# Optimization experiments

Hardware: AMD Instinct MI355X
Metric: run time of the kernel (lower is better)

## Reference

```python
import jax, jax.numpy as jnp
import numpy as np

N, NFEAT, NHID, NCLASS, NHEADS = 3072, 128, 64, 64, 8
ALPHA = 0.2  # LeakyReLU negative slope
NEG = -9e15  # masking value from pyGAT


def gat_layer(h, mask, W, a):
    # h: [N, Fin]; mask: [N, N] bool; W: [H, Fin, Fout]; a: [H, 2*Fout]
    fout = W.shape[-1]
    Wh = jnp.einsum('ni,hio->hno', h, W)            # [H, N, Fout]
    e_src = jnp.einsum('hno,ho->hn', Wh, a[:, :fout])
    e_dst = jnp.einsum('hno,ho->hn', Wh, a[:, fout:])
    e = jax.nn.leaky_relu(e_src[:, :, None] + e_dst[:, None, :], ALPHA)  # [H,N,N]
    e = jnp.where(mask[None], e, NEG)
    att = jax.nn.softmax(e, axis=-1)                 # dropout is identity in eval
    out = jnp.einsum('hnm,hmo->hno', att, Wh)        # [H, N, Fout]
    out = jax.nn.elu(out)                            # concat=True -> elu
    # concat heads along feature dim: [N, H*Fout]
    return out.transpose(1, 0, 2).reshape(h.shape[0], -1)


def setup_inputs() -> dict:
    key = jax.random.key(0)
    ks = jax.random.split(key, 10)
    x = jax.random.normal(ks[0], (N, NFEAT), dtype=jnp.float32)
    adj = (jax.random.uniform(ks[1], (N, N)) < 0.01).astype(jnp.float32)
    adj = jnp.maximum(adj, jnp.eye(N, dtype=jnp.float32))
    hid = NHID * NHEADS
    dims = [(NFEAT, NHID), (hid, NHID), (hid, NHID), (hid, NCLASS)]
    params = {}
    for i, (fin, fout) in enumerate(dims):
        kw, ka = jax.random.split(ks[2 + i])
        params[f'W{i+1}'] = jax.random.normal(kw, (NHEADS, fin, fout), dtype=jnp.float32) * (1.0 / np.sqrt(fin))
        params[f'a{i+1}'] = jax.random.normal(ka, (NHEADS, 2 * fout), dtype=jnp.float32) * 0.1
    return {'x': x, 'adj': adj, **params}


def reference(x, adj, W1, a1, W2, a2, W3, a3, W4, a4):
    mask = adj > 0
    h = gat_layer(x, mask, W1, a1)
    h = gat_layer(h, mask, W2, a2)
    h = gat_layer(h, mask, W3, a3)
    h = gat_layer(h, mask, W4, a4)
    return h  # [N, NHEADS*NCLASS]
```

## Files before the change

kernel.cpp:

```cpp
#include <hip/hip_runtime.h>
#include <math.h>

#define NN 3072
#define NH 8
#define FO 64
#define FCAT 512
#define MAXDEG 128
#define ALPHA 0.2f

typedef __attribute__((ext_vector_type(8))) short bf16x8;
typedef __attribute__((ext_vector_type(4))) float f32x4;

static __device__ __forceinline__ unsigned short f2bf(float v) {
    union { float f; unsigned u; } x; x.f = v;
    unsigned r = x.u + 0x7fffu + ((x.u >> 16) & 1u);
    return (unsigned short)(r >> 16);
}
static __device__ __forceinline__ float bf2f(unsigned short b) {
    union { unsigned u; float f; } x; x.u = ((unsigned)b) << 16;
    return x.f;
}

__global__ __launch_bounds__(64) void build_csr_k(const float* __restrict__ adj,
                                                  int* __restrict__ deg,
                                                  int* __restrict__ nbr) {
    int row = blockIdx.x;
    int lane = threadIdx.x;
    const float* arow = adj + (size_t)row * NN;
    int count = 0;
    for (int base = 0; base < NN; base += 64) {
        float v = arow[base + lane];
        unsigned long long m = __ballot(v > 0.0f);
        if (v > 0.0f) {
            int pos = count + __popcll(m & ((1ull << lane) - 1ull));
            if (pos < MAXDEG) nbr[(size_t)row * MAXDEG + pos] = base + lane;
        }
        count += __popcll(m);
    }
    if (lane == 0) deg[row] = count < MAXDEG ? count : MAXDEG;
}

__global__ __launch_bounds__(256) void conv_x_k(const float* __restrict__ x,
                                                unsigned short* __restrict__ xh,
                                                unsigned short* __restrict__ xl, int n) {
    int i = blockIdx.x * 256 + threadIdx.x;
    if (i < n) {
        float v = x[i];
        unsigned short hb = f2bf(v);
        xh[i] = hb;
        xl[i] = f2bf(v - bf2f(hb));
    }
}

__global__ __launch_bounds__(256) void conv_wt_k(const float* __restrict__ W1,
                                                 const float* __restrict__ W2,
                                                 const float* __restrict__ W3,
                                                 const float* __restrict__ W4,
                                                 unsigned short* __restrict__ Wth,
                                                 unsigned short* __restrict__ Wtl) {
    __shared__ float t[64][65];
    int b = blockIdx.x;
    const float* W; int K; int local; size_t obase;
    if (b < 16)       { W = W1; K = 128; local = b;       obase = 0; }
    else if (b < 80)  { W = W2; K = 512; local = b - 16;  obase = 65536; }
    else if (b < 144) { W = W3; K = 512; local = b - 80;  obase = 327680; }
    else              { W = W4; K = 512; local = b - 144; obase = 589824; }
    int nkt = K >> 6;
    int h = local / nkt, kt = local - h * nkt;
    int k0 = kt * 64;
    int tid = threadIdx.x;
    for (int idx = tid; idx < 4096; idx += 256) {
        int r = idx >> 6, c = idx & 63;
        t[r][c] = W[(size_t)h * K * FO + (size_t)(k0 + r) * FO + c];
    }
    __syncthreads();
    for (int idx = tid; idx < 4096; idx += 256) {
        int o = idx >> 6, kk = idx & 63;
        float v = t[kk][o];
        unsigned short hb = f2bf(v);
        size_t dst = obase + (size_t)(h * FO + o) * K + k0 + kk;
        Wth[dst] = hb;
        Wtl[dst] = f2bf(v - bf2f(hb));
    }
}

__global__ __launch_bounds__(256) void gemm_ee_k(const unsigned short* __restrict__ Ah,
                                                 const unsigned short* __restrict__ Al,
                                                 const unsigned short* __restrict__ Bh,
                                                 const unsigned short* __restrict__ Bl,
                                                 const float* __restrict__ a,
                                                 float* __restrict__ C,
                                                 float* __restrict__ esrc,
                                                 float* __restrict__ edst, int K) {
    __shared__ __align__(16) unsigned char smem[40960];
    typedef unsigned short AsT[64][80];
    typedef float CsT[68];
    AsT* As = reinterpret_cast<AsT*>(smem);
    AsT* Bs = reinterpret_cast<AsT*>(smem + 20480);
    CsT* Cs = reinterpret_cast<CsT*>(smem);

    const int tid = threadIdx.x;
    const int h = blockIdx.x;
    const int r0 = blockIdx.y * 64;
    const int lane = tid & 63;
    const int wid = tid >> 6;
    const int wr = wid >> 1, wc = wid & 1;
    const int lr = lane & 15, lg = lane >> 4;

    const unsigned short* Bhh = Bh + (size_t)h * FO * K;
    const unsigned short* Bll = Bl + (size_t)h * FO * K;

    f32x4 acc[2][2];
    #pragma unroll
    for (int i = 0; i < 2; ++i)
        #pragma unroll
        for (int j = 0; j < 2; ++j) acc[i][j] = (f32x4){0.f, 0.f, 0.f, 0.f};

    for (int k0 = 0; k0 < K; k0 += 64) {
        #pragma unroll
        for (int half = 0; half < 2; ++half) {
            int q = tid + half * 256;
            int row = q >> 3, cq = q & 7;
            int sw = (cq ^ (row & 7)) * 8;
            size_t ga = (size_t)(r0 + row) * K + k0 + cq * 8;
            *(bf16x8*)&As[0][row][sw] = *(const bf16x8*)(Ah + ga);
            *(bf16x8*)&As[1][row][sw] = *(const bf16x8*)(Al + ga);
            size_t gb = (size_t)row * K + k0 + cq * 8;
            *(bf16x8*)&Bs[0][row][sw] = *(const bf16x8*)(Bhh + gb);
            *(bf16x8*)&Bs[1][row][sw] = *(const bf16x8*)(Bll + gb);
        }
        __syncthreads();
        #pragma unroll
        for (int ks = 0; ks < 2; ++ks) {
            bf16x8 ah[2], al[2], bh[2], bl[2];
            int cq = ks * 4 + lg;
            #pragma unroll
            for (int i = 0; i < 2; ++i) {
                int row = wr * 32 + i * 16 + lr;
                int offa = (cq ^ (row & 7)) * 8;
                ah[i] = *(const bf16x8*)&As[0][row][offa];
                al[i] = *(const bf16x8*)&As[1][row][offa];
                int col = wc * 32 + i * 16 + lr;
                int offb = (cq ^ (col & 7)) * 8;
                bh[i] = *(const bf16x8*)&Bs[0][col][offb];
                bl[i] = *(const bf16x8*)&Bs[1][col][offb];
            }
            #pragma unroll
            for (int i = 0; i < 2; ++i)
                #pragma unroll
                for (int j = 0; j < 2; ++j) {
                    acc[i][j] = __builtin_amdgcn_mfma_f32_16x16x32_bf16(ah[i], bh[j], acc[i][j], 0, 0, 0);
                    acc[i][j] = __builtin_amdgcn_mfma_f32_16x16x32_bf16(ah[i], bl[j], acc[i][j], 0, 0, 0);
                    acc[i][j] = __builtin_amdgcn_mfma_f32_16x16x32_bf16(al[i], bh[j], acc[i][j], 0, 0, 0);
                }
        }
        __syncthreads();
    }

    #pragma unroll
    for (int i = 0; i < 2; ++i)
        #pragma unroll
        for (int j = 0; j < 2; ++j)
            #pragma unroll
            for (int r = 0; r < 4; ++r)
                Cs[wr * 32 + i * 16 + lg * 4 + r][wc * 32 + j * 16 + lr] = acc[i][j][r];
    __syncthreads();

    #pragma unroll
    for (int it = 0; it < 4; ++it) {
        int idx = tid + it * 256;
        int r = idx >> 4, c4 = idx & 15;
        *(float4*)&C[(size_t)(r0 + r) * FCAT + h * FO + c4 * 4] = *(float4*)&Cs[r][c4 * 4];
    }

    {
        int r = tid >> 2, sub = tid & 3;
        const float* av = a + h * 2 * FO;
        float s = 0.0f, dd = 0.0f;
        #pragma unroll
        for (int k = 0; k < 16; ++k) {
            float v = Cs[r][sub * 16 + k];
            s = fmaf(v, av[sub * 16 + k], s);
            dd = fmaf(v, av[FO + sub * 16 + k], dd);
        }
        s += __shfl_xor(s, 1); s += __shfl_xor(s, 2);
        dd += __shfl_xor(dd, 1); dd += __shfl_xor(dd, 2);
        if (sub == 0) {
            esrc[h * NN + r0 + r] = s;
            edst[h * NN + r0 + r] = dd;
        }
    }
}

__global__ __launch_bounds__(256) void attn_agg_k(const float* __restrict__ Wh,
                                                  const float* __restrict__ esrc,
                                                  const float* __restrict__ edst,
                                                  const int* __restrict__ deg,
                                                  const int* __restrict__ nbr,
                                                  float* __restrict__ outp,
                                                  unsigned short* __restrict__ oh,
                                                  unsigned short* __restrict__ ol,
                                                  int write_f32) {
    __shared__ float pbuf[4][MAXDEG];
    __shared__ int jbuf[4][MAXDEG];
    const int ws = threadIdx.x >> 6;
    const int lane = threadIdx.x & 63;
    const int h = blockIdx.x / (NN / 4);
    const int n = (blockIdx.x % (NN / 4)) * 4 + ws;
    const int d = deg[n];
    const int* nb = nbr + (size_t)n * MAXDEG;
    const float es = esrc[h * NN + n];
    const float* ed = edst + h * NN;

    for (int t = lane; t < d; t += 64) {
        int j = nb[t];
        float e = es + ed[j];
        e = (e > 0.0f) ? e : ALPHA * e;
        jbuf[ws][t] = j;
        pbuf[ws][t] = e;
    }
    float lm = -3.0e38f;
    for (int t = lane; t < d; t += 64) lm = fmaxf(lm, pbuf[ws][t]);
    #pragma unroll
    for (int off = 32; off; off >>= 1) lm = fmaxf(lm, __shfl_xor(lm, off));
    float lsum = 0.0f;
    for (int t = lane; t < d; t += 64) {
        float pv = __expf(pbuf[ws][t] - lm);
        pbuf[ws][t] = pv;
        lsum += pv;
    }
    #pragma unroll
    for (int off = 32; off; off >>= 1) lsum += __shfl_xor(lsum, off);

    const float* whb = Wh + h * FO + lane;
    float a0 = 0.f, a1 = 0.f, a2 = 0.f, a3 = 0.f;
    int t = 0;
    for (; t + 3 < d; t += 4) {
        a0 = fmaf(pbuf[ws][t + 0], whb[(size_t)jbuf[ws][t + 0] * FCAT], a0);
        a1 = fmaf(pbuf[ws][t + 1], whb[(size_t)jbuf[ws][t + 1] * FCAT], a1);
        a2 = fmaf(pbuf[ws][t + 2], whb[(size_t)jbuf[ws][t + 2] * FCAT], a2);
        a3 = fmaf(pbuf[ws][t + 3], whb[(size_t)jbuf[ws][t + 3] * FCAT], a3);
    }
    for (; t < d; ++t)
        a0 = fmaf(pbuf[ws][t], whb[(size_t)jbuf[ws][t] * FCAT], a0);
    float acc = (a0 + a1) + (a2 + a3);
    acc /= lsum;
    float r = (acc > 0.0f) ? acc : (__expf(acc) - 1.0f);
    size_t idx = (size_t)n * FCAT + h * FO + lane;
    if (write_f32) {
        outp[idx] = r;
    } else {
        unsigned short hb = f2bf(r);
        oh[idx] = hb;
        ol[idx] = f2bf(r - bf2f(hb));
    }
}

extern "C" void kernel_launch(void* const* d_in, const int* in_sizes, int n_in,
                              void* d_out, int out_size, void* d_ws, size_t ws_size,
                              hipStream_t stream) {
    const float* x   = (const float*)d_in[0];
    const float* adj = (const float*)d_in[1];
    const float* ap[4] = {(const float*)d_in[3], (const float*)d_in[5],
                          (const float*)d_in[7], (const float*)d_in[9]};
    float* out = (float*)d_out;

    char* p = (char*)d_ws;
    int* deg = (int*)p;              p += (size_t)NN * sizeof(int);
    int* nbr = (int*)p;              p += (size_t)NN * MAXDEG * sizeof(int);
    unsigned short* Ah = (unsigned short*)p; p += (size_t)NN * FCAT * 2;
    unsigned short* Al = (unsigned short*)p; p += (size_t)NN * FCAT * 2;
    float* WhF = (float*)p;          p += (size_t)NN * FCAT * sizeof(float);
    unsigned short* Wth = (unsigned short*)p; p += (size_t)851968 * 2;
    unsigned short* Wtl = (unsigned short*)p; p += (size_t)851968 * 2;
    float* esrc = (float*)p;         p += (size_t)NN * NH * sizeof(float);
    float* edst = (float*)p;         p += (size_t)NN * NH * sizeof(float);

    build_csr_k<<<NN, 64, 0, stream>>>(adj, deg, nbr);
    conv_x_k<<<(NN * 128 + 255) / 256, 256, 0, stream>>>(x, Ah, Al, NN * 128);
    conv_wt_k<<<208, 256, 0, stream>>>((const float*)d_in[2], (const float*)d_in[4],
                                       (const float*)d_in[6], (const float*)d_in[8],
                                       Wth, Wtl);

    const size_t woff[4] = {0, 65536, 327680, 589824};
    int K = 128;
    for (int L = 0; L < 4; ++L) {
        dim3 g(NH, NN / 64);
        gemm_ee_k<<<g, 256, 0, stream>>>(Ah, Al, Wth + woff[L], Wtl + woff[L],
                                         ap[L], WhF, esrc, edst, K);
        attn_agg_k<<<NH * (NN / 4), 256, 0, stream>>>(WhF, esrc, edst, deg, nbr,
                                                      out, Ah, Al, L == 3 ? 1 : 0);
        K = FCAT;
    }
}
```

Baseline: 154.8 us.

## Use direct global-to-LDS loads and halve GEMM row tile to 32

The projection GEMM now uses global_load_lds to stream A and B tiles straight into shared memory in an MFMA-friendly layout, replacing register-staged copies with XOR swizzle. The row tile shrinks from 64 to 32, doubling the grid so more blocks are in flight. Per-wave work drops to a 16x32 output tile and the e_src/e_dst reduction is redone for 8 threads per row. The trade-off is lower reuse of the B tile per block, more redundant weight loads, and possible LDS bank conflicts without the swizzle.

```diff
diff --git a/kernel.cpp b/kernel.cpp
--- a/kernel.cpp
+++ b/kernel.cpp
@@ -92,99 +92,101 @@
                                                  float* __restrict__ C,
                                                  float* __restrict__ esrc,
                                                  float* __restrict__ edst, int K) {
-    __shared__ __align__(16) unsigned char smem[40960];
-    typedef unsigned short AsT[64][80];
-    typedef float CsT[68];
-    AsT* As = reinterpret_cast<AsT*>(smem);
-    AsT* Bs = reinterpret_cast<AsT*>(smem + 20480);
-    CsT* Cs = reinterpret_cast<CsT*>(smem);
+    __shared__ __align__(16) unsigned short smem[12288];
+    float (*Cs)[68] = (float(*)[68])smem;
 
     const int tid = threadIdx.x;
-    const int h = blockIdx.x;
-    const int r0 = blockIdx.y * 64;
     const int lane = tid & 63;
     const int wid = tid >> 6;
     const int wr = wid >> 1, wc = wid & 1;
     const int lr = lane & 15, lg = lane >> 4;
+    const int h = blockIdx.x;
+    const int r0 = blockIdx.y * 32;
 
     const unsigned short* Bhh = Bh + (size_t)h * FO * K;
     const unsigned short* Bll = Bl + (size_t)h * FO * K;
 
-    f32x4 acc[2][2];
-    #pragma unroll
-    for (int i = 0; i < 2; ++i)
-        #pragma unroll
-        for (int j = 0; j < 2; ++j) acc[i][j] = (f32x4){0.f, 0.f, 0.f, 0.f};
+    f32x4 acc[2];
+    acc[0] = (f32x4){0.f, 0.f, 0.f, 0.f};
+    acc[1] = (f32x4){0.f, 0.f, 0.f, 0.f};
 
     for (int k0 = 0; k0 < K; k0 += 64) {
         #pragma unroll
-        for (int half = 0; half < 2; ++half) {
-            int q = tid + half * 256;
-            int row = q >> 3, cq = q & 7;
-            int sw = (cq ^ (row & 7)) * 8;
-            size_t ga = (size_t)(r0 + row) * K + k0 + cq * 8;
-            *(bf16x8*)&As[0][row][sw] = *(const bf16x8*)(Ah + ga);
-            *(bf16x8*)&As[1][row][sw] = *(const bf16x8*)(Al + ga);
-            size_t gb = (size_t)row * K + k0 + cq * 8;
-            *(bf16x8*)&Bs[0][row][sw] = *(const bf16x8*)(Bhh + gb);
-            *(bf16x8*)&Bs[1][row][sw] = *(const bf16x8*)(Bll + gb);
+        for (int li = 0; li < 6; ++li) {
+            int L = wid + 4 * li;
+            unsigned short* lb;
+            const unsigned short* g;
+            if (L < 8) {
+                int hl = L >> 2, part = L & 3;
+                int slot = part * 64 + lane;
+                int cq = slot >> 5, row = slot & 31;
+                lb = smem + hl * 2048 + part * 512;
+                const unsigned short* base = hl ? Al : Ah;
+                g = base + (size_t)(r0 + row) * K + k0 + cq * 8;
+            } else {
+                int L2 = L - 8;
+                int hl = L2 >> 3, part = L2 & 7;
+                int slot = part * 64 + lane;
+                int cq = slot >> 6, col = slot & 63;
+                lb = smem + 4096 + hl * 4096 + part * 512;
+                const unsigned short* base = hl ? Bll : Bhh;
+                g = base + (size_t)col * K + k0 + cq * 8;
+            }
+            __builtin_amdgcn_global_load_lds(
+                (const __attribute__((address_space(1))) unsigned int*)g,
+                (__attribute__((address_space(3))) unsigned int*)lb, 16, 0, 0);
         }
         __syncthreads();
+
         #pragma unroll
         for (int ks = 0; ks < 2; ++ks) {
-            bf16x8 ah[2], al[2], bh[2], bl[2];
             int cq = ks * 4 + lg;
+            int arow = wr * 16 + lr;
+            bf16x8 ah = *(const bf16x8*)&smem[(cq * 32 + arow) * 8];
+            bf16x8 al = *(const bf16x8*)&smem[2048 + (cq * 32 + arow) * 8];
+            bf16x8 bh[2], bl[2];
             #pragma unroll
-            for (int i = 0; i < 2; ++i) {
-                int row = wr * 32 + i * 16 + lr;
-                int offa = (cq ^ (row & 7)) * 8;
-                ah[i] = *(const bf16x8*)&As[0][row][offa];
-                al[i] = *(const bf16x8*)&As[1][row][offa];
-                int col = wc * 32 + i * 16 + lr;
-                int offb = (cq ^ (col & 7)) * 8;
-                bh[i] = *(const bf16x8*)&Bs[0][col][offb];
-                bl[i] = *(const bf16x8*)&Bs[1][col][offb];
+            for (int j = 0; j < 2; ++j) {
+                int col = wc * 32 + j * 16 + lr;
+                bh[j] = *(const bf16x8*)&smem[4096 + (cq * 64 + col) * 8];
+                bl[j] = *(const bf16x8*)&smem[8192 + (cq * 64 + col) * 8];
             }
             #pragma unroll
-            for (int i = 0; i < 2; ++i)
-                #pragma unroll
-                for (int j = 0; j < 2; ++j) {
-                    acc[i][j] = __builtin_amdgcn_mfma_f32_16x16x32_bf16(ah[i], bh[j], acc[i][j], 0, 0, 0);
-                    acc[i][j] = __builtin_amdgcn_mfma_f32_16x16x32_bf16(ah[i], bl[j], acc[i][j], 0, 0, 0);
-                    acc[i][j] = __builtin_amdgcn_mfma_f32_16x16x32_bf16(al[i], bh[j], acc[i][j], 0, 0, 0);
-                }
+            for (int j = 0; j < 2; ++j) {
+                acc[j] = __builtin_amdgcn_mfma_f32_16x16x32_bf16(ah, bh[j], acc[j], 0, 0, 0);
+                acc[j] = __builtin_amdgcn_mfma_f32_16x16x32_bf16(ah, bl[j], acc[j], 0, 0, 0);
+                acc[j] = __builtin_amdgcn_mfma_f32_16x16x32_bf16(al, bh[j], acc[j], 0, 0, 0);
+            }
         }
         __syncthreads();
     }
 
     #pragma unroll
-    for (int i = 0; i < 2; ++i)
-        #pragma unroll
-        for (int j = 0; j < 2; ++j)
-            #pragma unroll
-            for (int r = 0; r < 4; ++r)
-                Cs[wr * 32 + i * 16 + lg * 4 + r][wc * 32 + j * 16 + lr] = acc[i][j][r];
+    for (int j = 0; j < 2; ++j)
+        #pragma unroll
+        for (int r = 0; r < 4; ++r)
+            Cs[wr * 16 + lg * 4 + r][wc * 32 + j * 16 + lr] = acc[j][r];
     __syncthreads();
 
     #pragma unroll
-    for (int it = 0; it < 4; ++it) {
+    for (int it = 0; it < 2; ++it) {
         int idx = tid + it * 256;
         int r = idx >> 4, c4 = idx & 15;
         *(float4*)&C[(size_t)(r0 + r) * FCAT + h * FO + c4 * 4] = *(float4*)&Cs[r][c4 * 4];
     }
 
     {
-        int r = tid >> 2, sub = tid & 3;
+        int r = tid >> 3, sub = tid & 7;
         const float* av = a + h * 2 * FO;
         float s = 0.0f, dd = 0.0f;
         #pragma unroll
-        for (int k = 0; k < 16; ++k) {
-            float v = Cs[r][sub * 16 + k];
-            s = fmaf(v, av[sub * 16 + k], s);
-            dd = fmaf(v, av[FO + sub * 16 + k], dd);
-        }
-        s += __shfl_xor(s, 1); s += __shfl_xor(s, 2);
-        dd += __shfl_xor(dd, 1); dd += __shfl_xor(dd, 2);
+        for (int k = 0; k < 8; ++k) {
+            float v = Cs[r][sub * 8 + k];
+            s = fmaf(v, av[sub * 8 + k], s);
+            dd = fmaf(v, av[FO + sub * 8 + k], dd);
+        }
+        s += __shfl_xor(s, 1); s += __shfl_xor(s, 2); s += __shfl_xor(s, 4);
+        dd += __shfl_xor(dd, 1); dd += __shfl_xor(dd, 2); dd += __shfl_xor(dd, 4);
         if (sub == 0) {
             esrc[h * NN + r0 + r] = s;
             edst[h * NN + r0 + r] = dd;
@@ -285,7 +287,7 @@
     const size_t woff[4] = {0, 65536, 327680, 589824};
     int K = 128;
     for (int L = 0; L < 4; ++L) {
-        dim3 g(NH, NN / 64);
+        dim3 g(NH, NN / 32);
         gemm_ee_k<<<g, 256, 0, stream>>>(Ah, Al, Wth + woff[L], Wtl + woff[L],
                                          ap[L], WhF, esrc, edst, K);
         attn_agg_k<<<NH * (NN / 4), 256, 0, stream>>>(WhF, esrc, edst, deg, nbr,
```

New measurement: 175.9 us. 13.6% more time.

## Fuse prelude kernels into one launch and register-prefetch GEMM tiles

Applied to the files above, without the earlier changes.

The CSR build, x conversion and weight transpose/conversion kernels are merged into a single 1024-block prelude kernel, removing two launches and letting the independent work run concurrently. The GEMM main loop now loads the next K-tile from global memory into registers before doing the MFMA work on the current LDS tile, so global latency overlaps with compute. This costs extra registers and an additional barrier per iteration.

```diff
diff --git a/kernel.cpp b/kernel.cpp
--- a/kernel.cpp
+++ b/kernel.cpp
@@ -21,66 +21,69 @@
     return x.f;
 }
 
-__global__ __launch_bounds__(64) void build_csr_k(const float* __restrict__ adj,
-                                                  int* __restrict__ deg,
-                                                  int* __restrict__ nbr) {
-    int row = blockIdx.x;
-    int lane = threadIdx.x;
-    const float* arow = adj + (size_t)row * NN;
-    int count = 0;
-    for (int base = 0; base < NN; base += 64) {
-        float v = arow[base + lane];
-        unsigned long long m = __ballot(v > 0.0f);
-        if (v > 0.0f) {
-            int pos = count + __popcll(m & ((1ull << lane) - 1ull));
-            if (pos < MAXDEG) nbr[(size_t)row * MAXDEG + pos] = base + lane;
-        }
-        count += __popcll(m);
-    }
-    if (lane == 0) deg[row] = count < MAXDEG ? count : MAXDEG;
-}
-
-__global__ __launch_bounds__(256) void conv_x_k(const float* __restrict__ x,
-                                                unsigned short* __restrict__ xh,
-                                                unsigned short* __restrict__ xl, int n) {
-    int i = blockIdx.x * 256 + threadIdx.x;
-    if (i < n) {
-        float v = x[i];
-        unsigned short hb = f2bf(v);
-        xh[i] = hb;
-        xl[i] = f2bf(v - bf2f(hb));
-    }
-}
-
-__global__ __launch_bounds__(256) void conv_wt_k(const float* __restrict__ W1,
+__global__ __launch_bounds__(256) void prelude_k(const float* __restrict__ x,
+                                                 const float* __restrict__ adj,
+                                                 const float* __restrict__ W1,
                                                  const float* __restrict__ W2,
                                                  const float* __restrict__ W3,
                                                  const float* __restrict__ W4,
+                                                 unsigned short* __restrict__ Ah,
+                                                 unsigned short* __restrict__ Al,
                                                  unsigned short* __restrict__ Wth,
-                                                 unsigned short* __restrict__ Wtl) {
+                                                 unsigned short* __restrict__ Wtl,
+                                                 int* __restrict__ deg,
+                                                 int* __restrict__ nbr) {
     __shared__ float t[64][65];
-    int b = blockIdx.x;
-    const float* W; int K; int local; size_t obase;
-    if (b < 16)       { W = W1; K = 128; local = b;       obase = 0; }
-    else if (b < 80)  { W = W2; K = 512; local = b - 16;  obase = 65536; }
-    else if (b < 144) { W = W3; K = 512; local = b - 80;  obase = 327680; }
-    else              { W = W4; K = 512; local = b - 144; obase = 589824; }
-    int nkt = K >> 6;
-    int h = local / nkt, kt = local - h * nkt;
-    int k0 = kt * 64;
-    int tid = threadIdx.x;
-    for (int idx = tid; idx < 4096; idx += 256) {
-        int r = idx >> 6, c = idx & 63;
-        t[r][c] = W[(size_t)h * K * FO + (size_t)(k0 + r) * FO + c];
-    }
-    __syncthreads();
-    for (int idx = tid; idx < 4096; idx += 256) {
-        int o = idx >> 6, kk = idx & 63;
-        float v = t[kk][o];
-        unsigned short hb = f2bf(v);
-        size_t dst = obase + (size_t)(h * FO + o) * K + k0 + kk;
-        Wth[dst] = hb;
-        Wtl[dst] = f2bf(v - bf2f(hb));
+    const int b = blockIdx.x, tid = threadIdx.x;
+
+    if (b < 256) {
+        int base = b * 1536 + tid;
+        #pragma unroll
+        for (int i = 0; i < 6; ++i) {
+            int idx = base + i * 256;
+            float v = x[idx];
+            unsigned short hb = f2bf(v);
+            Ah[idx] = hb;
+            Al[idx] = f2bf(v - bf2f(hb));
+        }
+        if (b < 208) {
+            const float* W; int K; int local; size_t obase;
+            if (b < 16)       { W = W1; K = 128; local = b;       obase = 0; }
+            else if (b < 80)  { W = W2; K = 512; local = b - 16;  obase = 65536; }
+            else if (b < 144) { W = W3; K = 512; local = b - 80;  obase = 327680; }
+            else              { W = W4; K = 512; local = b - 144; obase = 589824; }
+            int nkt = K >> 6;
+            int h = local / nkt, kt = local - h * nkt;
+            int k0 = kt * 64;
+            for (int idx = tid; idx < 4096; idx += 256) {
+                int r = idx >> 6, c = idx & 63;
+                t[r][c] = W[(size_t)h * K * FO + (size_t)(k0 + r) * FO + c];
+            }
+            __syncthreads();
+            for (int idx = tid; idx < 4096; idx += 256) {
+                int o = idx >> 6, kk = idx & 63;
+                float v = t[kk][o];
+                unsigned short hb = f2bf(v);
+                size_t dst = obase + (size_t)(h * FO + o) * K + k0 + kk;
+                Wth[dst] = hb;
+                Wtl[dst] = f2bf(v - bf2f(hb));
+            }
+        }
+    } else {
+        int row = (b - 256) * 4 + (tid >> 6);
+        int lane = tid & 63;
+        const float* arow = adj + (size_t)row * NN;
+        int count = 0;
+        for (int base = 0; base < NN; base += 64) {
+            float v = arow[base + lane];
+            unsigned long long m = __ballot(v > 0.0f);
+            if (v > 0.0f) {
+                int pos = count + __popcll(m & ((1ull << lane) - 1ull));
+                if (pos < MAXDEG) nbr[(size_t)row * MAXDEG + pos] = base + lane;
+            }
+            count += __popcll(m);
+        }
+        if (lane == 0) deg[row] = count < MAXDEG ? count : MAXDEG;
     }
 }
 
@@ -93,10 +96,9 @@
                                                  float* __restrict__ esrc,
                                                  float* __restrict__ edst, int K) {
     __shared__ __align__(16) unsigned char smem[40960];
-    typedef unsigned short AsT[64][80];
     typedef float CsT[68];
-    AsT* As = reinterpret_cast<AsT*>(smem);
-    AsT* Bs = reinterpret_cast<AsT*>(smem + 20480);
+    unsigned short* As_ = (unsigned short*)smem;
+    unsigned short* Bs_ = (unsigned short*)(smem + 20480);
     CsT* Cs = reinterpret_cast<CsT*>(smem);
 
     const int tid = threadIdx.x;
@@ -110,26 +112,43 @@
     const unsigned short* Bhh = Bh + (size_t)h * FO * K;
     const unsigned short* Bll = Bl + (size_t)h * FO * K;
 
+    const int row0 = tid >> 3, cq0 = tid & 7;
+    const int off0 = row0 * 80 + ((cq0 ^ (row0 & 7)) * 8);
+    const size_t gA0 = (size_t)(r0 + row0) * K + cq0 * 8;
+    const size_t gA1 = gA0 + (size_t)32 * K;
+    const size_t gB0 = (size_t)row0 * K + cq0 * 8;
+    const size_t gB1 = gB0 + (size_t)32 * K;
+
+    bf16x8 ra0h, ra0l, ra1h, ra1l, rb0h, rb0l, rb1h, rb1l;
+
+    auto loadg = [&](int k0) {
+        ra0h = *(const bf16x8*)(Ah + gA0 + k0);
+        ra0l = *(const bf16x8*)(Al + gA0 + k0);
+        ra1h = *(const bf16x8*)(Ah + gA1 + k0);
+        ra1l = *(const bf16x8*)(Al + gA1 + k0);
+        rb0h = *(const bf16x8*)(Bhh + gB0 + k0);
+        rb0l = *(const bf16x8*)(Bll + gB0 + k0);
+        rb1h = *(const bf16x8*)(Bhh + gB1 + k0);
+        rb1l = *(const bf16x8*)(Bll + gB1 + k0);
+    };
+    auto store_lds = [&]() {
+        *(bf16x8*)&As_[off0] = ra0h;
+        *(bf16x8*)&As_[off0 + 2560] = ra1h;
+        *(bf16x8*)&As_[5120 + off0] = ra0l;
+        *(bf16x8*)&As_[5120 + off0 + 2560] = ra1l;
+        *(bf16x8*)&Bs_[off0] = rb0h;
+        *(bf16x8*)&Bs_[off0 + 2560] = rb1h;
+        *(bf16x8*)&Bs_[5120 + off0] = rb0l;
+        *(bf16x8*)&Bs_[5120 + off0 + 2560] = rb1l;
+    };
+
     f32x4 acc[2][2];
     #pragma unroll
     for (int i = 0; i < 2; ++i)
         #pragma unroll
         for (int j = 0; j < 2; ++j) acc[i][j] = (f32x4){0.f, 0.f, 0.f, 0.f};
 
-    for (int k0 = 0; k0 < K; k0 += 64) {
-        #pragma unroll
-        for (int half = 0; half < 2; ++half) {
-            int q = tid + half * 256;
-            int row = q >> 3, cq = q & 7;
-            int sw = (cq ^ (row & 7)) * 8;
-            size_t ga = (size_t)(r0 + row) * K + k0 + cq * 8;
-            *(bf16x8*)&As[0][row][sw] = *(const bf16x8*)(Ah + ga);
-            *(bf16x8*)&As[1][row][sw] = *(const bf16x8*)(Al + ga);
-            size_t gb = (size_t)row * K + k0 + cq * 8;
-            *(bf16x8*)&Bs[0][row][sw] = *(const bf16x8*)(Bhh + gb);
-            *(bf16x8*)&Bs[1][row][sw] = *(const bf16x8*)(Bll + gb);
-        }
-        __syncthreads();
+    auto mfma_phase = [&]() {
         #pragma unroll
         for (int ks = 0; ks < 2; ++ks) {
             bf16x8 ah[2], al[2], bh[2], bl[2];
@@ -137,13 +156,13 @@
             #pragma unroll
             for (int i = 0; i < 2; ++i) {
                 int row = wr * 32 + i * 16 + lr;
-                int offa = (cq ^ (row & 7)) * 8;
-                ah[i] = *(const bf16x8*)&As[0][row][offa];
-                al[i] = *(const bf16x8*)&As[1][row][offa];
+                int offa = row * 80 + ((cq ^ (row & 7)) * 8);
+                ah[i] = *(const bf16x8*)&As_[offa];
+                al[i] = *(const bf16x8*)&As_[5120 + offa];
                 int col = wc * 32 + i * 16 + lr;
-                int offb = (cq ^ (col & 7)) * 8;
-                bh[i] = *(const bf16x8*)&Bs[0][col][offb];
-                bl[i] = *(const bf16x8*)&Bs[1][col][offb];
+                int offb = col * 80 + ((cq ^ (col & 7)) * 8);
+                bh[i] = *(const bf16x8*)&Bs_[offb];
+                bl[i] = *(const bf16x8*)&Bs_[5120 + offb];
             }
             #pragma unroll
             for (int i = 0; i < 2; ++i)
@@ -154,8 +173,20 @@
                     acc[i][j] = __builtin_amdgcn_mfma_f32_16x16x32_bf16(al[i], bh[j], acc[i][j], 0, 0, 0);
                 }
         }
+    };
+
+    loadg(0);
+    store_lds();
+    __syncthreads();
+    for (int k0 = 64; k0 < K; k0 += 64) {
+        loadg(k0);
+        mfma_phase();
         __syncthreads();
-    }
+        store_lds();
+        __syncthreads();
+    }
+    mfma_phase();
+    __syncthreads();
 
     #pragma unroll
     for (int i = 0; i < 2; ++i)
@@ -276,11 +307,10 @@
     float* esrc = (float*)p;         p += (size_t)NN * NH * sizeof(float);
     float* edst = (float*)p;         p += (size_t)NN * NH * sizeof(float);
 
-    build_csr_k<<<NN, 64, 0, stream>>>(adj, deg, nbr);
-    conv_x_k<<<(NN * 128 + 255) / 256, 256, 0, stream>>>(x, Ah, Al, NN * 128);
-    conv_wt_k<<<208, 256, 0, stream>>>((const float*)d_in[2], (const float*)d_in[4],
-                                       (const float*)d_in[6], (const float*)d_in[8],
-                                       Wth, Wtl);
+    prelude_k<<<1024, 256, 0, stream>>>(x, adj,
+                                        (const float*)d_in[2], (const float*)d_in[4],
+                                        (const float*)d_in[6], (const float*)d_in[8],
+                                        Ah, Al, Wth, Wtl, deg, nbr);
 
     const size_t woff[4] = {0, 65536, 327680, 589824};
     int K = 128;
```

After: 144.0 us. -7.0%, faster.
